# Kernel tuning notes

Measured on AMD Instinct MI355X. Metric: run time of the kernel, lower is better.

The kernel has to match this reference:

```python
import jax, jax.numpy as jnp
import numpy as np
from jax import nn as jnn

N = 100000      # nodes
E = 3200000     # edges (avg degree 32)
G = 1024        # graphs in batch
F_IN = 3        # num_features (hard-coded in module)
D = 32          # dim (hard-coded in module)
BN_EPS = 1e-5


def setup_inputs() -> dict:
    key = jax.random.key(0)
    ks = jax.random.split(key, 24)
    def lin(k, i, o):
        return (jax.random.normal(k, (i, o), jnp.float32) / np.sqrt(i)).astype(jnp.float32)
    inp = {}
    inp["x"] = jax.random.normal(ks[0], (N, F_IN), jnp.float32)
    inp["edge_index"] = jax.random.randint(ks[1], (2, E), 0, N, dtype=jnp.int32)
    inp["batch"] = jnp.sort(jax.random.randint(ks[2], (N,), 0, G, dtype=jnp.int32))
    idx = 3
    in_dims = [F_IN, D, D]
    for l in (1, 2, 3):
        inp[f"W{l}a"] = lin(ks[idx], in_dims[l - 1], D); idx += 1
        inp[f"b{l}a"] = jnp.zeros((D,), jnp.float32)
        inp[f"W{l}b"] = lin(ks[idx], D, D); idx += 1
        inp[f"b{l}b"] = jnp.zeros((D,), jnp.float32)
        inp[f"g{l}"] = jnp.ones((D,), jnp.float32)            # BN gamma
        inp[f"be{l}"] = jnp.zeros((D,), jnp.float32)          # BN beta
        inp[f"m{l}"] = 0.1 * jax.random.normal(ks[idx], (D,), jnp.float32); idx += 1  # running mean
        inp[f"v{l}"] = jax.random.uniform(ks[idx], (D,), jnp.float32, 0.5, 1.5); idx += 1  # running var
    inp["Wf1"] = lin(ks[idx], D, D); idx += 1
    inp["bf1"] = jnp.zeros((D,), jnp.float32)
    inp["Wf2"] = lin(ks[idx], D, 1)
    inp["bf2"] = jnp.zeros((1,), jnp.float32)
    return inp


def reference(x, edge_index, batch,
              W1a, b1a, W1b, b1b, g1, be1, m1, v1,
              W2a, b2a, W2b, b2b, g2, be2, m2, v2,
              W3a, b3a, W3b, b3b, g3, be3, m3, v3,
              Wf1, bf1, Wf2, bf2):
    src, dst = edge_index[0], edge_index[1]

    def gin_bn(h, Wa, ba, Wb, bb, g, be, m, v):
        # GINConv (eps=0): nn(x + sum_{j->i} x_j); then relu; then BatchNorm1d (eval stats)
        agg = jax.ops.segment_sum(h[src], dst, num_segments=N) + h  # [N, d]
        h2 = jnn.relu(agg @ Wa + ba) @ Wb + bb                      # 2-layer MLP
        h2 = jnn.relu(h2)
        return g * (h2 - m) * jax.lax.rsqrt(v + BN_EPS) + be

    h = gin_bn(x, W1a, b1a, W1b, b1b, g1, be1, m1, v1)
    h = gin_bn(h, W2a, b2a, W2b, b2b, g2, be2, m2, v2)
    h = gin_bn(h, W3a, b3a, W3b, b3b, g3, be3, m3, v3)
    p = jax.ops.segment_sum(h, batch, num_segments=G)   # global_add_pool -> [G, D]
    p = jnn.relu(p @ Wf1 + bf1)
    # dropout p=0.5 is identity at inference
    return jnp.tanh(p @ Wf2 + bf2)                      # [G, 1]
```

## Files before the change

### kernel.cpp

```cpp
#include <hip/hip_runtime.h>
#include <math.h>

#define D 32
#define BN_EPS 1e-5f
#define NRANGE 512
#define RWC 196
#define MAXD 80
#define EPB 8192
#define K1_TPB 512
#define EPT (EPB / K1_TPB)
#define PCH 8

__global__ __launch_bounds__(K1_TPB) void build_part(
    const int* __restrict__ src, const int* __restrict__ dst,
    unsigned int* __restrict__ part, int* __restrict__ gcount,
    int E, int cap, int RW, unsigned long long M) {
    __shared__ unsigned int sorted[EPB];
    __shared__ unsigned short rid[EPB];
    __shared__ int cnt[NRANGE];
    __shared__ int exc[NRANGE];
    __shared__ int cur[NRANGE];
    __shared__ int gbase[NRANGE];
    int t = threadIdx.x;
    cnt[t] = 0;
    __syncthreads();

    int base = blockIdx.x * EPB;
    int n = min(EPB, E - base);

    unsigned int mypk[EPT];
    unsigned short myr[EPT];
#pragma unroll
    for (int k = 0; k < EPT; k++) {
        int i = t + k * K1_TPB;
        if (i < n) {
            int d = dst[base + i];
            int s = src[base + i];
            int r = (int)(((unsigned long long)d * M) >> 40);
            mypk[k] = ((unsigned)(d - r * RW) << 17) | (unsigned)s;
            myr[k] = (unsigned short)r;
            atomicAdd(&cnt[r], 1);
        } else myr[k] = 0xFFFFu;
    }
    __syncthreads();

    int inc = cnt[t];
    exc[t] = inc;
    __syncthreads();
    for (int s = 1; s < NRANGE; s <<= 1) {
        int u = (t >= s) ? exc[t - s] : 0;
        __syncthreads();
        exc[t] += u;
        __syncthreads();
    }
    int excl = exc[t] - cnt[t];
    __syncthreads();
    exc[t] = excl;
    cur[t] = excl;
    gbase[t] = atomicAdd(&gcount[t], cnt[t]);
    __syncthreads();

#pragma unroll
    for (int k = 0; k < EPT; k++) {
        if (myr[k] != 0xFFFFu) {
            int j = atomicAdd(&cur[myr[k]], 1);
            sorted[j] = mypk[k];
            rid[j] = myr[k];
        }
    }
    __syncthreads();

    for (int j = t; j < n; j += K1_TPB) {
        int r = rid[j];
        int pos = gbase[r] + (j - exc[r]);
        if (pos < cap) part[(size_t)r * cap + pos] = sorted[j];
    }
}

__global__ __launch_bounds__(1024) void build_csr(
    const unsigned int* __restrict__ part, const int* __restrict__ gcount,
    int* __restrict__ col, int* __restrict__ deg,
    int cap, int RW, int N, int maxd) {
    __shared__ int bucket[RWC * MAXD];
    __shared__ int rank_[RWC];
    int r = blockIdx.x, t = threadIdx.x, T = blockDim.x;
    for (int i = t; i < RW; i += T) rank_[i] = 0;
    __syncthreads();

    int count = gcount[r]; if (count > cap) count = cap;
    const unsigned int* p = part + (size_t)r * cap;
    for (int i = t; i < count; i += T) {
        unsigned int v = p[i];
        int dl = (int)(v >> 17);
        int s = (int)(v & 0x1FFFFu);
        int slot = atomicAdd(&rank_[dl], 1);
        if (slot < maxd) bucket[dl * maxd + slot] = s;
    }
    __syncthreads();

    int nbase = r * RW;
    int nvalid = N - nbase; if (nvalid > RW) nvalid = RW;
    if (nvalid <= 0) return;
    int words = nvalid * maxd;
    int4* dst4 = (int4*)&col[(size_t)nbase * maxd];
    const int4* src4 = (const int4*)bucket;
    int nq = words >> 2;
    for (int i = t; i < nq; i += T) dst4[i] = src4[i];
    for (int i = t; i < nvalid; i += T) {
        int rk = rank_[i];
        deg[nbase + i] = rk < maxd ? rk : maxd;
    }
}

__global__ void compute_y(const float* __restrict__ x, const float* __restrict__ W1a,
                          float* __restrict__ y, int N) {
    long long gid = (long long)blockIdx.x * blockDim.x + threadIdx.x;
    int i = (int)(gid >> 5);
    int lane = (int)(gid & 31);
    if (i >= N) return;
    float x0 = x[i * 3 + 0], x1 = x[i * 3 + 1], x2 = x[i * 3 + 2];
    float t = x0 * W1a[0 * D + lane];
    t = fmaf(x1, W1a[1 * D + lane], t);
    t = fmaf(x2, W1a[2 * D + lane], t);
    y[(size_t)i * D + lane] = t;
}

template <bool SKIP_WA>
__global__ void layer_fused(const float* __restrict__ hin, const int* __restrict__ deg,
                            const int* __restrict__ col, int maxd,
                            const float* __restrict__ Wa, const float* __restrict__ ba,
                            const float* __restrict__ Wb, const float* __restrict__ bb,
                            const float* __restrict__ g, const float* __restrict__ be,
                            const float* __restrict__ m, const float* __restrict__ v,
                            float* __restrict__ hout, int N) {
    long long gid = (long long)blockIdx.x * blockDim.x + threadIdx.x;
    int i = (int)(gid >> 5);
    int lane = (int)(gid & 31);
    if (i >= N) return;

    float acc = hin[(size_t)i * D + lane];
    int dg = deg[i];
    if (dg > maxd) dg = maxd;
    const int* cp = &col[(size_t)i * maxd];
    int e = 0;
    for (; e + 16 <= dg; e += 16) {
        int4 c0 = *(const int4*)&cp[e];
        int4 c1 = *(const int4*)&cp[e + 4];
        int4 c2 = *(const int4*)&cp[e + 8];
        int4 c3 = *(const int4*)&cp[e + 12];
        float a0 = hin[(size_t)c0.x * D + lane];
        float a1 = hin[(size_t)c0.y * D + lane];
        float a2 = hin[(size_t)c0.z * D + lane];
        float a3 = hin[(size_t)c0.w * D + lane];
        float a4 = hin[(size_t)c1.x * D + lane];
        float a5 = hin[(size_t)c1.y * D + lane];
        float a6 = hin[(size_t)c1.z * D + lane];
        float a7 = hin[(size_t)c1.w * D + lane];
        float a8 = hin[(size_t)c2.x * D + lane];
        float a9 = hin[(size_t)c2.y * D + lane];
        float aa = hin[(size_t)c2.z * D + lane];
        float ab = hin[(size_t)c2.w * D + lane];
        float ac = hin[(size_t)c3.x * D + lane];
        float ad = hin[(size_t)c3.y * D + lane];
        float ae = hin[(size_t)c3.z * D + lane];
        float af = hin[(size_t)c3.w * D + lane];
        acc += ((a0 + a1) + (a2 + a3)) + ((a4 + a5) + (a6 + a7)) +
               (((a8 + a9) + (aa + ab)) + ((ac + ad) + (ae + af)));
    }
    for (; e + 4 <= dg; e += 4) {
        int4 c = *(const int4*)&cp[e];
        float a0 = hin[(size_t)c.x * D + lane];
        float a1 = hin[(size_t)c.y * D + lane];
        float a2 = hin[(size_t)c.z * D + lane];
        float a3 = hin[(size_t)c.w * D + lane];
        acc += (a0 + a1) + (a2 + a3);
    }
    for (; e < dg; e++) acc += hin[(size_t)cp[e] * D + lane];

    float t;
    if (SKIP_WA) {
        t = fmaxf(acc + ba[lane], 0.f);
    } else {
        t = ba[lane];
#pragma unroll
        for (int k = 0; k < D; k++) {
            float ak = __shfl(acc, k, D);
            t = fmaf(ak, Wa[k * D + lane], t);
        }
        t = fmaxf(t, 0.f);
    }
    float o = bb[lane];
#pragma unroll
    for (int j = 0; j < D; j++) {
        float tj = __shfl(t, j, D);
        o = fmaf(tj, Wb[j * D + lane], o);
    }
    o = fmaxf(o, 0.f);
    hout[(size_t)i * D + lane] =
        g[lane] * (o - m[lane]) * rsqrtf(v[lane] + BN_EPS) + be[lane];
}

__device__ __forceinline__ int lower_bound_i(const int* a, int n, int key) {
    int lo = 0, hi = n;
    while (lo < hi) {
        int mid = (lo + hi) >> 1;
        if (a[mid] < key) lo = mid + 1; else hi = mid;
    }
    return lo;
}

__global__ void pool_partial(const float* __restrict__ h, const int* __restrict__ batch,
                             float* __restrict__ pool, int N, int G) {
    long long gid = (long long)blockIdx.x * blockDim.x + threadIdx.x;
    int grp = (int)(gid >> 5);
    int lane = (int)(gid & 31);
    int gi = grp / PCH;
    int c = grp - gi * PCH;
    if (gi >= G) return;
    int lo = lower_bound_i(batch, N, gi);
    int hi = lower_bound_i(batch, N, gi + 1);
    int len = hi - lo;
    if (len <= 0) return;
    int chunk = (len + PCH - 1) / PCH;
    int s = lo + c * chunk;
    int e = s + chunk; if (e > hi) e = hi;
    if (s >= e) return;
    float p = 0.f;
    for (int n = s; n < e; n++) p += h[(size_t)n * D + lane];
    atomicAdd(&pool[(size_t)gi * D + lane], p);
}

__global__ void head_kernel(const float* __restrict__ pool, const float* __restrict__ Wf1,
                            const float* __restrict__ bf1, const float* __restrict__ Wf2,
                            const float* __restrict__ bf2, float* __restrict__ out, int G) {
    long long gid = (long long)blockIdx.x * blockDim.x + threadIdx.x;
    int gi = (int)(gid >> 5);
    int lane = (int)(gid & 31);
    if (gi >= G) return;
    float p = pool[(size_t)gi * D + lane];
    float q = bf1[lane];
#pragma unroll
    for (int j = 0; j < D; j++) {
        float pj = __shfl(p, j, D);
        q = fmaf(pj, Wf1[j * D + lane], q);
    }
    q = fmaxf(q, 0.f);
    float r = q * Wf2[lane];
#pragma unroll
    for (int off = 16; off; off >>= 1) r += __shfl_xor(r, off, D);
    if (lane == 0) out[gi] = tanhf(r + bf2[0]);
}

extern "C" void kernel_launch(void* const* d_in, const int* in_sizes, int n_in,
                              void* d_out, int out_size, void* d_ws, size_t ws_size,
                              hipStream_t stream) {
    const float* x = (const float*)d_in[0];
    const int* ei = (const int*)d_in[1];
    const int* batch = (const int*)d_in[2];
    const int E = in_sizes[1] / 2;
    const int N = in_sizes[2];
    const int G = out_size;
    const int* src = ei;
    const int* dst = ei + E;

    const float* P[3][8];
    for (int l = 0; l < 3; l++)
        for (int k = 0; k < 8; k++) P[l][k] = (const float*)d_in[3 + 8 * l + k];
    const float* Wf1 = (const float*)d_in[27];
    const float* bf1 = (const float*)d_in[28];
    const float* Wf2 = (const float*)d_in[29];
    const float* bf2 = (const float*)d_in[30];

    const int RW = (N + NRANGE - 1) / NRANGE;
    const unsigned long long M = ((1ull << 40) + RW - 1) / RW;
    int mean = (E + NRANGE - 1) / NRANGE;
    int cap = mean + mean / 8 + 64;
    cap = (cap + 7) & ~7;

    float* ws = (float*)d_ws;
    size_t off = 0;
    float* h0 = ws + off; off += (size_t)N * D;
    float* h1 = ws + off; off += (size_t)N * D;
    unsigned int* part = (unsigned int*)h0;
    int* deg = (int*)(ws + off); off += N;
    int* gcount = (int*)(ws + off); off += NRANGE;
    float* pool = ws + off; off += (size_t)G * D;
    int* col = (int*)(ws + off);
    size_t remaining = ws_size / 4 > off ? ws_size / 4 - off : 0;
    int maxd = (int)(remaining / (size_t)N);
    if (maxd > MAXD) maxd = MAXD;
    maxd &= ~3;
    if (maxd < 4) maxd = 4;

    const int B = 256;
    long long tN32 = (long long)N * D;
    int nbp = (E + EPB - 1) / EPB;

    hipMemsetAsync(gcount, 0, NRANGE * sizeof(int), stream);
    build_part<<<nbp, K1_TPB, 0, stream>>>(src, dst, part, gcount, E, cap, RW, M);
    build_csr<<<NRANGE, 1024, 0, stream>>>(part, gcount, col, deg, cap, RW, N, maxd);

    compute_y<<<(int)((tN32 + B - 1) / B), B, 0, stream>>>(x, P[0][0], h0, N);
    layer_fused<true><<<(int)((tN32 + B - 1) / B), B, 0, stream>>>(
        h0, deg, col, maxd, P[0][0], P[0][1], P[0][2], P[0][3],
        P[0][4], P[0][5], P[0][6], P[0][7], h1, N);

    layer_fused<false><<<(int)((tN32 + B - 1) / B), B, 0, stream>>>(
        h1, deg, col, maxd, P[1][0], P[1][1], P[1][2], P[1][3],
        P[1][4], P[1][5], P[1][6], P[1][7], h0, N);

    layer_fused<false><<<(int)((tN32 + B - 1) / B), B, 0, stream>>>(
        h0, deg, col, maxd, P[2][0], P[2][1], P[2][2], P[2][3],
        P[2][4], P[2][5], P[2][6], P[2][7], h1, N);

    hipMemsetAsync(pool, 0, (size_t)G * D * sizeof(float), stream);
    pool_partial<<<(int)(((long long)G * PCH * 32 + B - 1) / B), B, 0, stream>>>(
        h1, batch, pool, N, G);
    head_kernel<<<(int)(((long long)G * D + B - 1) / B), B, 0, stream>>>(
        pool, Wf1, bf1, Wf2, bf2, (float*)d_out, G);
}
```

Measured before the change: 375.3 us.

## Pad CSR rows with self-indices, shuffle-broadcast neighbor ids, fuse compute_y into build_csr

Each adjacency row is padded to a multiple of 16 with the node's own index, and the self term is scaled to cancel the padding. This lets the gather loop run in fixed 16-wide batches with no scalar tail. Neighbor indices are loaded once per wave lane and broadcast with shuffles instead of every lane reading int4 vectors. The first-layer projection is folded into the CSR build kernel, and the two memsets are merged into one, which removes launches. The partition buffer now gets its own workspace region and maxd is rounded to 16, which costs extra workspace and wasted gathers on padded slots.

```diff
diff --git a/kernel.cpp b/kernel.cpp
--- a/kernel.cpp
+++ b/kernel.cpp
@@ -80,6 +80,7 @@
 __global__ __launch_bounds__(1024) void build_csr(
     const unsigned int* __restrict__ part, const int* __restrict__ gcount,
     int* __restrict__ col, int* __restrict__ deg,
+    const float* __restrict__ x, const float* __restrict__ W1a, float* __restrict__ y,
     int cap, int RW, int N, int maxd) {
     __shared__ int bucket[RWC * MAXD];
     __shared__ int rank_[RWC];
@@ -89,16 +90,23 @@
 
     int count = gcount[r]; if (count > cap) count = cap;
     const unsigned int* p = part + (size_t)r * cap;
+    int nbase = r * RW;
     for (int i = t; i < count; i += T) {
         unsigned int v = p[i];
         int dl = (int)(v >> 17);
-        int s = (int)(v & 0x1FFFFu);
         int slot = atomicAdd(&rank_[dl], 1);
-        if (slot < maxd) bucket[dl * maxd + slot] = s;
-    }
-    __syncthreads();
-
-    int nbase = r * RW;
+        if (slot < maxd) bucket[dl * maxd + slot] = (int)(v & 0x1FFFFu);
+    }
+    __syncthreads();
+
+    for (int i = t; i < RW; i += T) {
+        int rk = rank_[i]; if (rk > maxd) rk = maxd;
+        int pdg = (rk + 15) & ~15; if (pdg > maxd) pdg = maxd;
+        int self = nbase + i;
+        for (int k = rk; k < pdg; k++) bucket[i * maxd + k] = self;
+    }
+    __syncthreads();
+
     int nvalid = N - nbase; if (nvalid > RW) nvalid = RW;
     if (nvalid <= 0) return;
     int words = nvalid * maxd;
@@ -110,19 +118,54 @@
         int rk = rank_[i];
         deg[nbase + i] = rk < maxd ? rk : maxd;
     }
-}
-
-__global__ void compute_y(const float* __restrict__ x, const float* __restrict__ W1a,
-                          float* __restrict__ y, int N) {
-    long long gid = (long long)blockIdx.x * blockDim.x + threadIdx.x;
-    int i = (int)(gid >> 5);
-    int lane = (int)(gid & 31);
-    if (i >= N) return;
-    float x0 = x[i * 3 + 0], x1 = x[i * 3 + 1], x2 = x[i * 3 + 2];
-    float t = x0 * W1a[0 * D + lane];
-    t = fmaf(x1, W1a[1 * D + lane], t);
-    t = fmaf(x2, W1a[2 * D + lane], t);
-    y[(size_t)i * D + lane] = t;
+
+    int gidx = t >> 5, lane = t & 31;
+    for (int nl = gidx; nl < nvalid; nl += 32) {
+        int node = nbase + nl;
+        float x0 = x[node * 3 + 0], x1 = x[node * 3 + 1], x2 = x[node * 3 + 2];
+        float tv = x0 * W1a[0 * D + lane];
+        tv = fmaf(x1, W1a[1 * D + lane], tv);
+        tv = fmaf(x2, W1a[2 * D + lane], tv);
+        y[(size_t)node * D + lane] = tv;
+    }
+}
+
+__device__ __forceinline__ float gsum16(const float* __restrict__ hin, int creg, int off,
+                                        int lane) {
+    int i0 = __shfl(creg, off + 0, 32);
+    int i1 = __shfl(creg, off + 1, 32);
+    int i2 = __shfl(creg, off + 2, 32);
+    int i3 = __shfl(creg, off + 3, 32);
+    int i4 = __shfl(creg, off + 4, 32);
+    int i5 = __shfl(creg, off + 5, 32);
+    int i6 = __shfl(creg, off + 6, 32);
+    int i7 = __shfl(creg, off + 7, 32);
+    int i8 = __shfl(creg, off + 8, 32);
+    int i9 = __shfl(creg, off + 9, 32);
+    int i10 = __shfl(creg, off + 10, 32);
+    int i11 = __shfl(creg, off + 11, 32);
+    int i12 = __shfl(creg, off + 12, 32);
+    int i13 = __shfl(creg, off + 13, 32);
+    int i14 = __shfl(creg, off + 14, 32);
+    int i15 = __shfl(creg, off + 15, 32);
+    float a0 = hin[(size_t)i0 * D + lane];
+    float a1 = hin[(size_t)i1 * D + lane];
+    float a2 = hin[(size_t)i2 * D + lane];
+    float a3 = hin[(size_t)i3 * D + lane];
+    float a4 = hin[(size_t)i4 * D + lane];
+    float a5 = hin[(size_t)i5 * D + lane];
+    float a6 = hin[(size_t)i6 * D + lane];
+    float a7 = hin[(size_t)i7 * D + lane];
+    float a8 = hin[(size_t)i8 * D + lane];
+    float a9 = hin[(size_t)i9 * D + lane];
+    float a10 = hin[(size_t)i10 * D + lane];
+    float a11 = hin[(size_t)i11 * D + lane];
+    float a12 = hin[(size_t)i12 * D + lane];
+    float a13 = hin[(size_t)i13 * D + lane];
+    float a14 = hin[(size_t)i14 * D + lane];
+    float a15 = hin[(size_t)i15 * D + lane];
+    return ((((a0 + a1) + (a2 + a3)) + ((a4 + a5) + (a6 + a7))) +
+            (((a8 + a9) + (a10 + a11)) + ((a12 + a13) + (a14 + a15))));
 }
 
 template <bool SKIP_WA>
@@ -138,44 +181,25 @@
     int lane = (int)(gid & 31);
     if (i >= N) return;
 
-    float acc = hin[(size_t)i * D + lane];
     int dg = deg[i];
     if (dg > maxd) dg = maxd;
+    int pdg = (dg + 15) & ~15; if (pdg > maxd) pdg = maxd;
+    float acc = hin[(size_t)i * D + lane] * (float)(1 + dg - pdg);
     const int* cp = &col[(size_t)i * maxd];
-    int e = 0;
-    for (; e + 16 <= dg; e += 16) {
-        int4 c0 = *(const int4*)&cp[e];
-        int4 c1 = *(const int4*)&cp[e + 4];
-        int4 c2 = *(const int4*)&cp[e + 8];
-        int4 c3 = *(const int4*)&cp[e + 12];
-        float a0 = hin[(size_t)c0.x * D + lane];
-        float a1 = hin[(size_t)c0.y * D + lane];
-        float a2 = hin[(size_t)c0.z * D + lane];
-        float a3 = hin[(size_t)c0.w * D + lane];
-        float a4 = hin[(size_t)c1.x * D + lane];
-        float a5 = hin[(size_t)c1.y * D + lane];
-        float a6 = hin[(size_t)c1.z * D + lane];
-        float a7 = hin[(size_t)c1.w * D + lane];
-        float a8 = hin[(size_t)c2.x * D + lane];
-        float a9 = hin[(size_t)c2.y * D + lane];
-        float aa = hin[(size_t)c2.z * D + lane];
-        float ab = hin[(size_t)c2.w * D + lane];
-        float ac = hin[(size_t)c3.x * D + lane];
-        float ad = hin[(size_t)c3.y * D + lane];
-        float ae = hin[(size_t)c3.z * D + lane];
-        float af = hin[(size_t)c3.w * D + lane];
-        acc += ((a0 + a1) + (a2 + a3)) + ((a4 + a5) + (a6 + a7)) +
-               (((a8 + a9) + (aa + ab)) + ((ac + ad) + (ae + af)));
-    }
-    for (; e + 4 <= dg; e += 4) {
-        int4 c = *(const int4*)&cp[e];
-        float a0 = hin[(size_t)c.x * D + lane];
-        float a1 = hin[(size_t)c.y * D + lane];
-        float a2 = hin[(size_t)c.z * D + lane];
-        float a3 = hin[(size_t)c.w * D + lane];
-        acc += (a0 + a1) + (a2 + a3);
-    }
-    for (; e < dg; e++) acc += hin[(size_t)cp[e] * D + lane];
+
+    int cA = cp[lane];
+    int cB = 0, cC = 0;
+    if (pdg > 32) cB = cp[32 + lane];
+    if (pdg > 64) cC = cp[64 + (lane & 15)];
+
+    float s = 0.f;
+    if (pdg >= 32) s += gsum16(hin, cA, 0, lane) + gsum16(hin, cA, 16, lane);
+    if (pdg >= 64) s += gsum16(hin, cB, 0, lane) + gsum16(hin, cB, 16, lane);
+    if (pdg & 16) {
+        int creg = (pdg == 16) ? cA : ((pdg == 48) ? cB : cC);
+        s += gsum16(hin, creg, 0, lane);
+    }
+    acc += s;
 
     float t;
     if (SKIP_WA) {
@@ -281,7 +305,7 @@
     size_t off = 0;
     float* h0 = ws + off; off += (size_t)N * D;
     float* h1 = ws + off; off += (size_t)N * D;
-    unsigned int* part = (unsigned int*)h0;
+    unsigned int* part = (unsigned int*)(ws + off); off += (size_t)NRANGE * cap;
     int* deg = (int*)(ws + off); off += N;
     int* gcount = (int*)(ws + off); off += NRANGE;
     float* pool = ws + off; off += (size_t)G * D;
@@ -289,18 +313,18 @@
     size_t remaining = ws_size / 4 > off ? ws_size / 4 - off : 0;
     int maxd = (int)(remaining / (size_t)N);
     if (maxd > MAXD) maxd = MAXD;
-    maxd &= ~3;
-    if (maxd < 4) maxd = 4;
+    maxd &= ~15;
+    if (maxd < 16) maxd = 16;
 
     const int B = 256;
     long long tN32 = (long long)N * D;
     int nbp = (E + EPB - 1) / EPB;
 
-    hipMemsetAsync(gcount, 0, NRANGE * sizeof(int), stream);
+    hipMemsetAsync(gcount, 0, (NRANGE + (size_t)G * D) * sizeof(int), stream);
     build_part<<<nbp, K1_TPB, 0, stream>>>(src, dst, part, gcount, E, cap, RW, M);
-    build_csr<<<NRANGE, 1024, 0, stream>>>(part, gcount, col, deg, cap, RW, N, maxd);
-
-    compute_y<<<(int)((tN32 + B - 1) / B), B, 0, stream>>>(x, P[0][0], h0, N);
+    build_csr<<<NRANGE, 1024, 0, stream>>>(part, gcount, col, deg, x, P[0][0], h0,
+                                           cap, RW, N, maxd);
+
     layer_fused<true><<<(int)((tN32 + B - 1) / B), B, 0, stream>>>(
         h0, deg, col, maxd, P[0][0], P[0][1], P[0][2], P[0][3],
         P[0][4], P[0][5], P[0][6], P[0][7], h1, N);
@@ -313,7 +337,6 @@
         h0, deg, col, maxd, P[2][0], P[2][1], P[2][2], P[2][3],
         P[2][4], P[2][5], P[2][6], P[2][7], h1, N);
 
-    hipMemsetAsync(pool, 0, (size_t)G * D * sizeof(float), stream);
     pool_partial<<<(int)(((long long)G * PCH * 32 + B - 1) / B), B, 0, stream>>>(
         h1, batch, pool, N, G);
     head_kernel<<<(int)(((long long)G * D + B - 1) / B), B, 0, stream>>>(
```

Measured after the change: 351.3 us. -6.4%, faster.
